# Optimization experiments

Measured on AMD Instinct MI355X. Metric: run time of the kernel, lower is better.

## Reference

```python
import jax, jax.numpy as jnp
import numpy as np

# Mamba-1.4B-like dims
BATCH, SEQ, HID = 1, 2048, 2048
INTER, STATE, DT_RANK, KCONV = 4096, 16, 128, 4


def setup_inputs() -> dict:
    key = jax.random.key(0)
    ks = jax.random.split(key, 8)
    f = jnp.float32
    return {
        "input_states": jax.random.normal(ks[0], (BATCH, SEQ, HID), f),
        "in_proj_w": jax.random.normal(ks[1], (HID, 2 * INTER), f) * (HID ** -0.5),
        "conv_w": jax.random.normal(ks[2], (INTER, 1, KCONV), f) * (KCONV ** -0.5),  # (O, I/groups=1, K) depthwise
        "conv_b": jnp.zeros((INTER,), f),
        "x_proj_w": jax.random.normal(ks[3], (INTER, DT_RANK + 2 * STATE), f) * (INTER ** -0.5),
        "dt_proj_w": jax.random.normal(ks[4], (DT_RANK, INTER), f) * (DT_RANK ** -0.5),
        "dt_proj_b": jax.random.normal(ks[5], (INTER,), f) * 0.1,
        "A_log": jnp.log(jnp.broadcast_to(jnp.arange(1, STATE + 1, dtype=f), (INTER, STATE))),
        "D": jnp.ones((INTER,), f),
        "out_proj_w": jax.random.normal(ks[6], (INTER, HID), f) * (INTER ** -0.5),
    }


def _mamba_forward(input_states, in_proj_w, conv_w, conv_b, x_proj_w,
                   dt_proj_w, dt_proj_b, A_log, D, out_proj_w):
    Bsz, L, _ = input_states.shape
    Idim, _, K = conv_w.shape
    N = A_log.shape[1]
    R = dt_proj_w.shape[0]

    proj = input_states @ in_proj_w                       # (B, L, 2I)
    hidden, gate = jnp.split(proj, 2, axis=-1)            # each (B, L, I)

    # depthwise causal conv over sequence (pad K-1, keep first L outputs)
    xc = jnp.swapaxes(hidden, 1, 2)                       # (B, I, L)
    xc = jax.lax.conv_general_dilated(
        xc, conv_w, window_strides=(1,), padding=((K - 1, K - 1),),
        feature_group_count=Idim)
    xc = xc[:, :, :L] + conv_b[None, :, None]
    u = jax.nn.silu(jnp.swapaxes(xc, 1, 2))               # (B, L, I)

    # input-dependent SSM params
    ssm_in = u @ x_proj_w                                 # (B, L, R + 2N)
    dt_in, Bc, Cc = jnp.split(ssm_in, [R, R + N], axis=-1)
    dt = jax.nn.softplus(dt_in @ dt_proj_w + dt_proj_b)   # (B, L, I)
    A = -jnp.exp(A_log)                                   # (I, N)

    def step(state, xs):
        dt_t, B_t, C_t, u_t = xs                          # (B,I) (B,N) (B,N) (B,I)
        dA = jnp.exp(dt_t[:, :, None] * A[None])          # (B, I, N)
        state = state * dA + (dt_t * u_t)[:, :, None] * B_t[:, None, :]
        y_t = jnp.einsum('bin,bn->bi', state, C_t)
        return state, y_t

    xs = (jnp.swapaxes(dt, 0, 1), jnp.swapaxes(Bc, 0, 1),
          jnp.swapaxes(Cc, 0, 1), jnp.swapaxes(u, 0, 1))
    state0 = jnp.zeros((Bsz, Idim, N), dt.dtype)
    _, ys = jax.lax.scan(step, state0, xs)                # (L, B, I)
    y = jnp.swapaxes(ys, 0, 1)                            # (B, L, I)

    y = (y + u * D) * jax.nn.silu(gate)
    return y @ out_proj_w                                 # (B, L, H)


def reference(input_states, in_proj_w, conv_w, conv_b, x_proj_w,
              dt_proj_w, dt_proj_b, A_log, D, out_proj_w):
    return _mamba_forward(input_states, in_proj_w, conv_w, conv_b, x_proj_w,
                          dt_proj_w, dt_proj_b, A_log, D, out_proj_w)
```

## Files before the change

kernel.cpp:

```cpp
#include <hip/hip_runtime.h>
#include <stdint.h>

#define LSEQ 2048
#define HID  2048
#define IDIM 4096
#define NSTATE 16
#define RRANK 128
#define GDIM 160

#define GCHUNK 64
#define TCHUNK (LSEQ / GCHUNK)

typedef _Float16 f16x8 __attribute__((ext_vector_type(8)));
typedef float f32x4 __attribute__((ext_vector_type(4)));

#define GLOAD_LDS16(g, l) __builtin_amdgcn_global_load_lds( \
    (const __attribute__((address_space(1))) void*)(g),     \
    (__attribute__((address_space(3))) void*)(l), 16, 0, 0)

__global__ void f32_to_f16_kernel(const float* __restrict__ in, _Float16* __restrict__ out, int n) {
    int i = blockIdx.x * 256 + threadIdx.x;
    if (i < n) out[i] = (_Float16)in[i];
}

__global__ void transpose_f32_f16_kernel(const float* __restrict__ in, _Float16* __restrict__ out,
                                         int R, int C) {
    __shared__ float tile[32][33];
    int bx = blockIdx.x;
    int by = blockIdx.y;
    int tx = threadIdx.x & 31;
    int ty = threadIdx.x >> 5;
    int r0 = by * 32, c0 = bx * 32;
    #pragma unroll
    for (int j = 0; j < 32; j += 8)
        tile[ty + j][tx] = in[(long)(r0 + ty + j) * C + c0 + tx];
    __syncthreads();
    #pragma unroll
    for (int j = 0; j < 32; j += 8)
        out[(long)(c0 + ty + j) * R + r0 + tx] = (_Float16)tile[tx][ty + j];
}

#define BM 128
#define BK 64

template <typename CT, int BN_>
__global__ __launch_bounds__(256)
void gemm_bt_kernel(const _Float16* __restrict__ A, const _Float16* __restrict__ Bt,
                    CT* __restrict__ C, int M, int N, int K, int kc) {
    constexpr int NI = BN_ / 32;
    constexpr int NISS_B = BN_ * 8 / 256;
    __shared__ _Float16 As[BM * BK];
    __shared__ _Float16 Bs[BN_ * BK];
    const int m0 = blockIdx.y * BM;
    const int n0 = blockIdx.x * BN_;
    const int t = threadIdx.x;
    const int wave = t >> 6;
    const int lane = t & 63;
    const int wm = wave >> 1, wn = wave & 1;
    const int lrow = lane & 15;
    const int quad = lane >> 4;
    const int sw8 = (lrow & 7) * 8;

    f32x4 acc[4][NI];
    #pragma unroll
    for (int mi = 0; mi < 4; ++mi)
        #pragma unroll
        for (int ni = 0; ni < NI; ++ni)
            #pragma unroll
            for (int r = 0; r < 4; ++r)
                acc[mi][ni][r] = 0.f;

    long gA[4];
    #pragma unroll
    for (int j = 0; j < 4; ++j) {
        int s = j * 256 + t;
        int row = s >> 3;
        int ch = (s & 7) ^ (row & 7);
        gA[j] = (long)(m0 + row) * K + ch * 8;
    }
    long gB[NISS_B];
    #pragma unroll
    for (int j = 0; j < NISS_B; ++j) {
        int s = j * 256 + t;
        int row = s >> 3;
        int ch = (s & 7) ^ (row & 7);
        gB[j] = (long)(n0 + row) * K + ch * 8;
    }

    const int k_begin = blockIdx.z * kc;
    const int k_end = k_begin + kc;

    for (int kk = k_begin; kk < k_end; kk += BK) {
        #pragma unroll
        for (int j = 0; j < 4; ++j)
            GLOAD_LDS16(A + gA[j] + kk, As + (j * 256 + wave * 64) * 8);
        #pragma unroll
        for (int j = 0; j < NISS_B; ++j)
            GLOAD_LDS16(Bt + gB[j] + kk, Bs + (j * 256 + wave * 64) * 8);
        __syncthreads();

        #pragma unroll
        for (int h = 0; h < 2; ++h) {
            const int qoff = (h * 32 + quad * 8) ^ sw8;
            f16x8 af[4], bf[NI];
            #pragma unroll
            for (int mi = 0; mi < 4; ++mi)
                af[mi] = *(const f16x8*)(As + (wm * 64 + mi * 16 + lrow) * BK + qoff);
            #pragma unroll
            for (int ni = 0; ni < NI; ++ni)
                bf[ni] = *(const f16x8*)(Bs + (wn * (BN_ / 2) + ni * 16 + lrow) * BK + qoff);
            #pragma unroll
            for (int mi = 0; mi < 4; ++mi)
                #pragma unroll
                for (int ni = 0; ni < NI; ++ni)
                    acc[mi][ni] = __builtin_amdgcn_mfma_f32_16x16x32_f16(af[mi], bf[ni], acc[mi][ni], 0, 0, 0);
        }
        __syncthreads();
    }

    CT* Cz = C + (long)blockIdx.z * M * N;
    #pragma unroll
    for (int mi = 0; mi < 4; ++mi) {
        #pragma unroll
        for (int ni = 0; ni < NI; ++ni) {
            int col = n0 + wn * (BN_ / 2) + ni * 16 + lrow;
            if (col < N) {
                #pragma unroll
                for (int r = 0; r < 4; ++r) {
                    int row = m0 + wm * 64 + mi * 16 + quad * 4 + r;
                    Cz[(long)row * N + col] = (CT)acc[mi][ni][r];
                }
            }
        }
    }
}

__global__ void xproj_reduce_kernel(const float* __restrict__ part, float* __restrict__ ssm,
                                    _Float16* __restrict__ dtin) {
    int idx = blockIdx.x * 256 + threadIdx.x;
    if (idx >= LSEQ * GDIM) return;
    int t = idx / GDIM;
    int c = idx - t * GDIM;
    float v = 0.f;
    #pragma unroll
    for (int k = 0; k < 8; ++k)
        v += part[((long)k * LSEQ + t) * 256 + c];
    ssm[idx] = v;
    if (c < RRANK) dtin[t * RRANK + c] = (_Float16)v;
}

__global__ void conv_silu_kernel(const _Float16* __restrict__ proj, const float* __restrict__ w,
                                 const float* __restrict__ b, _Float16* __restrict__ u16) {
    int idx = blockIdx.x * 256 + threadIdx.x;
    int i0 = (idx & 511) * 8;
    int t0 = (idx >> 9) * 4;
    f16x8 r[7];
    #pragma unroll
    for (int k = 0; k < 7; ++k) {
        int tt = t0 - 3 + k;
        if (tt >= 0) r[k] = *(const f16x8*)(proj + (long)tt * (2 * IDIM) + i0);
        else         r[k] = f16x8{0,0,0,0,0,0,0,0};
    }
    float4 wv[8]; float bb[8];
    #pragma unroll
    for (int j = 0; j < 8; ++j) { wv[j] = ((const float4*)w)[i0 + j]; bb[j] = b[i0 + j]; }
    #pragma unroll
    for (int tt = 0; tt < 4; ++tt) {
        f16x8 res;
        #pragma unroll
        for (int j = 0; j < 8; ++j) {
            float a = bb[j] + (float)r[tt][j] * wv[j].x + (float)r[tt+1][j] * wv[j].y
                            + (float)r[tt+2][j] * wv[j].z + (float)r[tt+3][j] * wv[j].w;
            res[j] = (_Float16)(a / (1.f + __expf(-a)));
        }
        *(f16x8*)(u16 + (long)(t0 + tt) * IDIM + i0) = res;
    }
}

__device__ __forceinline__ float softplus_f(float x) {
    if (x > 20.f) return x;
    return log1pf(__expf(x));
}
__device__ __forceinline__ float silu_f(float x) {
    return x / (1.f + __expf(-x));
}

__global__ __launch_bounds__(256)
void scan_pass1_kernel(const _Float16* __restrict__ dtlin, const float* __restrict__ dtb,
                       const float* __restrict__ ssm, const _Float16* __restrict__ u16,
                       const float* __restrict__ A_log,
                       float* __restrict__ Pc, float* __restrict__ Sc) {
    const int c = blockIdx.y;
    const int i = blockIdx.x * 256 + threadIdx.x;

    __shared__ float Bs[TCHUNK * 16];
    for (int idx = threadIdx.x; idx < TCHUNK * 16; idx += 256) {
        int t = idx >> 4, n = idx & 15;
        Bs[idx] = ssm[(c * TCHUNK + t) * GDIM + RRANK + n];
    }
    __syncthreads();

    float A[16];
    {
        const float4* Ap = (const float4*)(A_log + i * 16);
        #pragma unroll
        for (int q = 0; q < 4; ++q) {
            float4 v = Ap[q];
            A[q * 4 + 0] = -__expf(v.x);
            A[q * 4 + 1] = -__expf(v.y);
            A[q * 4 + 2] = -__expf(v.z);
            A[q * 4 + 3] = -__expf(v.w);
        }
    }
    const float dtbi = dtb[i];

    float s[16], p[16];
    #pragma unroll
    for (int n = 0; n < 16; ++n) { s[n] = 0.f; p[n] = 1.f; }

    long base = (long)c * TCHUNK * IDIM + i;
    for (int t = 0; t < TCHUNK; ++t) {
        float dt = softplus_f((float)dtlin[base + (long)t * IDIM] + dtbi);
        float dtu = dt * (float)u16[base + (long)t * IDIM];
        #pragma unroll
        for (int n = 0; n < 16; ++n) {
            float dA = __expf(dt * A[n]);
            s[n] = s[n] * dA + dtu * Bs[t * 16 + n];
            p[n] *= dA;
        }
    }

    long o = ((long)c * IDIM + i) * 16;
    #pragma unroll
    for (int q = 0; q < 4; ++q) {
        *(float4*)(Pc + o + q * 4) = make_float4(p[q*4+0], p[q*4+1], p[q*4+2], p[q*4+3]);
        *(float4*)(Sc + o + q * 4) = make_float4(s[q*4+0], s[q*4+1], s[q*4+2], s[q*4+3]);
    }
}

__global__ void scan_combine_kernel(const float* __restrict__ Pc, float* __restrict__ ScInit) {
    int tid = blockIdx.x * 256 + threadIdx.x;
    const long stride = (long)IDIM * 16;
    float p4[4], s4[4];
    #pragma unroll
    for (int k = 0; k < 4; ++k) {
        p4[k] = Pc[(long)k * stride + tid];
        s4[k] = ScInit[(long)k * stride + tid];
    }
    float carry = 0.f;
    for (int g = 0; g < GCHUNK / 4; ++g) {
        float pc[4], sc[4];
        #pragma unroll
        for (int k = 0; k < 4; ++k) { pc[k] = p4[k]; sc[k] = s4[k]; }
        if (g + 1 < GCHUNK / 4) {
            #pragma unroll
            for (int k = 0; k < 4; ++k) {
                long o2 = (long)((g + 1) * 4 + k) * stride + tid;
                p4[k] = Pc[o2];
                s4[k] = ScInit[o2];
            }
        }
        #pragma unroll
        for (int k = 0; k < 4; ++k) {
            long o = (long)(g * 4 + k) * stride + tid;
            ScInit[o] = carry;
            carry = carry * pc[k] + sc[k];
        }
    }
}

__global__ __launch_bounds__(256)
void scan_pass3_kernel(const _Float16* __restrict__ dtlin, const float* __restrict__ dtb,
                       const float* __restrict__ ssm, const _Float16* __restrict__ u16,
                       const _Float16* __restrict__ proj, const float* __restrict__ A_log,
                       const float* __restrict__ Dp, const float* __restrict__ Init,
                       _Float16* __restrict__ y16) {
    const int c = blockIdx.y;
    const int i = blockIdx.x * 256 + threadIdx.x;

    __shared__ float Bs[TCHUNK * 16];
    __shared__ float Cs[TCHUNK * 16];
    for (int idx = threadIdx.x; idx < TCHUNK * 16; idx += 256) {
        int t = idx >> 4, n = idx & 15;
        Bs[idx] = ssm[(c * TCHUNK + t) * GDIM + RRANK + n];
        Cs[idx] = ssm[(c * TCHUNK + t) * GDIM + RRANK + NSTATE + n];
    }
    __syncthreads();

    float A[16];
    {
        const float4* Ap = (const float4*)(A_log + i * 16);
        #pragma unroll
        for (int q = 0; q < 4; ++q) {
            float4 v = Ap[q];
            A[q * 4 + 0] = -__expf(v.x);
            A[q * 4 + 1] = -__expf(v.y);
            A[q * 4 + 2] = -__expf(v.z);
            A[q * 4 + 3] = -__expf(v.w);
        }
    }
    const float dtbi = dtb[i];
    const float Dv = Dp[i];

    float s[16];
    {
        long o = ((long)c * IDIM + i) * 16;
        #pragma unroll
        for (int q = 0; q < 4; ++q) {
            float4 v = *(const float4*)(Init + o + q * 4);
            s[q*4+0] = v.x; s[q*4+1] = v.y; s[q*4+2] = v.z; s[q*4+3] = v.w;
        }
    }

    long base = (long)c * TCHUNK * IDIM + i;
    for (int t = 0; t < TCHUNK; ++t) {
        float dt = softplus_f((float)dtlin[base + (long)t * IDIM] + dtbi);
        float uv = (float)u16[base + (long)t * IDIM];
        float dtu = dt * uv;
        float y = 0.f;
        #pragma unroll
        for (int n = 0; n < 16; ++n) {
            float dA = __expf(dt * A[n]);
            s[n] = s[n] * dA + dtu * Bs[t * 16 + n];
            y += s[n] * Cs[t * 16 + n];
        }
        int tg = c * TCHUNK + t;
        float g = (float)proj[(long)tg * (2 * IDIM) + IDIM + i];
        float out = (y + uv * Dv) * silu_f(g);
        y16[base + (long)t * IDIM] = (_Float16)out;
    }
}

extern "C" void kernel_launch(void* const* d_in, const int* in_sizes, int n_in,
                              void* d_out, int out_size, void* d_ws, size_t ws_size,
                              hipStream_t stream) {
    const float* x_in  = (const float*)d_in[0];
    const float* w_in  = (const float*)d_in[1];
    const float* cw    = (const float*)d_in[2];
    const float* cb    = (const float*)d_in[3];
    const float* xw    = (const float*)d_in[4];
    const float* dtw   = (const float*)d_in[5];
    const float* dtb   = (const float*)d_in[6];
    const float* alog  = (const float*)d_in[7];
    const float* Dp    = (const float*)d_in[8];
    const float* ow    = (const float*)d_in[9];
    float* out = (float*)d_out;

    char* p = (char*)d_ws;
    auto alloc = [&](size_t bytes) { char* r = p; p += (bytes + 255) & ~255ull; return r; };
    _Float16* Xf    = (_Float16*)alloc((size_t)LSEQ * HID * 2);
    _Float16* Wt1   = (_Float16*)alloc((size_t)2 * IDIM * HID * 2);
    _Float16* proj  = (_Float16*)alloc((size_t)LSEQ * 2 * IDIM * 2);
    _Float16* u16   = (_Float16*)alloc((size_t)LSEQ * IDIM * 2);
    _Float16* Wt2   = (_Float16*)alloc((size_t)256 * IDIM * 2);
    float*    ssm   = (float*)alloc((size_t)LSEQ * GDIM * 4);
    _Float16* dtin  = (_Float16*)alloc((size_t)LSEQ * RRANK * 2);
    _Float16* Wt3   = (_Float16*)alloc((size_t)IDIM * RRANK * 2);
    _Float16* dtlin = (_Float16*)alloc((size_t)LSEQ * IDIM * 2);
    _Float16* Wt4   = (_Float16*)alloc((size_t)HID * IDIM * 2);
    _Float16* y16   = (_Float16*)alloc((size_t)LSEQ * IDIM * 2);

    float* xpart = (float*)Wt1;
    float* Pc = (float*)Wt1;
    float* Sc = Pc + (size_t)GCHUNK * IDIM * 16;

    f32_to_f16_kernel<<<(LSEQ * HID) / 256, 256, 0, stream>>>(x_in, Xf, LSEQ * HID);
    transpose_f32_f16_kernel<<<dim3(2 * IDIM / 32, HID / 32), 256, 0, stream>>>(w_in, Wt1, HID, 2 * IDIM);
    transpose_f32_f16_kernel<<<dim3(GDIM / 32, IDIM / 32), 256, 0, stream>>>(xw, Wt2, IDIM, GDIM);
    transpose_f32_f16_kernel<<<dim3(IDIM / 32, RRANK / 32), 256, 0, stream>>>(dtw, Wt3, RRANK, IDIM);
    transpose_f32_f16_kernel<<<dim3(HID / 32, IDIM / 32), 256, 0, stream>>>(ow, Wt4, IDIM, HID);

    gemm_bt_kernel<_Float16, 128><<<dim3(2 * IDIM / 128, LSEQ / BM, 1), 256, 0, stream>>>(
        Xf, Wt1, proj, LSEQ, 2 * IDIM, HID, HID);
    conv_silu_kernel<<<(LSEQ / 4) * (IDIM / 8) / 256, 256, 0, stream>>>(proj, cw, cb, u16);
    gemm_bt_kernel<float, 128><<<dim3(2, LSEQ / BM, 8), 256, 0, stream>>>(
        u16, Wt2, xpart, LSEQ, 256, IDIM, IDIM / 8);
    xproj_reduce_kernel<<<(LSEQ * GDIM + 255) / 256, 256, 0, stream>>>(xpart, ssm, dtin);
    gemm_bt_kernel<_Float16, 128><<<dim3(IDIM / 128, LSEQ / BM, 1), 256, 0, stream>>>(
        dtin, Wt3, dtlin, LSEQ, IDIM, RRANK, RRANK);
    scan_pass1_kernel<<<dim3(IDIM / 256, GCHUNK), 256, 0, stream>>>(
        dtlin, dtb, ssm, u16, alog, Pc, Sc);
    scan_combine_kernel<<<(IDIM * NSTATE) / 256, 256, 0, stream>>>(Pc, Sc);
    scan_pass3_kernel<<<dim3(IDIM / 256, GCHUNK), 256, 0, stream>>>(
        dtlin, dtb, ssm, u16, proj, alog, Dp, Sc, y16);
    gemm_bt_kernel<float, 64><<<dim3(HID / 64, LSEQ / BM, 1), 256, 0, stream>>>(
        y16, Wt4, out, LSEQ, HID, IDIM, IDIM);
}
```

Baseline: 519.7 us.

## Vectorize weight transpose, use pointer increments in GEMM, split-K out_proj

```diff
diff --git a/kernel.cpp b/kernel.cpp
--- a/kernel.cpp
+++ b/kernel.cpp
@@ -23,21 +23,58 @@
     if (i < n) out[i] = (_Float16)in[i];
 }
 
-__global__ void transpose_f32_f16_kernel(const float* __restrict__ in, _Float16* __restrict__ out,
-                                         int R, int C) {
-    __shared__ float tile[32][33];
-    int bx = blockIdx.x;
-    int by = blockIdx.y;
-    int tx = threadIdx.x & 31;
-    int ty = threadIdx.x >> 5;
-    int r0 = by * 32, c0 = bx * 32;
-    #pragma unroll
-    for (int j = 0; j < 32; j += 8)
-        tile[ty + j][tx] = in[(long)(r0 + ty + j) * C + c0 + tx];
-    __syncthreads();
-    #pragma unroll
-    for (int j = 0; j < 32; j += 8)
-        out[(long)(c0 + ty + j) * R + r0 + tx] = (_Float16)tile[tx][ty + j];
+__global__ __launch_bounds__(256)
+void transpose_f32_f16_kernel(const float* __restrict__ in, _Float16* __restrict__ out,
+                              int R, int C) {
+    __shared__ _Float16 tile[64][66];
+    const int c0 = blockIdx.x * 64, r0 = blockIdx.y * 64;
+    const int t = threadIdx.x;
+    const int tx = t & 15, ty = t >> 4;
+    const int ox = t & 7, oy = t >> 3;
+    const bool full = (c0 + 64 <= C) && (r0 + 64 <= R);
+    if (full) {
+        #pragma unroll
+        for (int j = 0; j < 4; ++j) {
+            int r = ty + j * 16;
+            float4 v = *(const float4*)(in + (long)(r0 + r) * C + c0 + tx * 4);
+            tile[r][tx * 4 + 0] = (_Float16)v.x;
+            tile[r][tx * 4 + 1] = (_Float16)v.y;
+            tile[r][tx * 4 + 2] = (_Float16)v.z;
+            tile[r][tx * 4 + 3] = (_Float16)v.w;
+        }
+        __syncthreads();
+        #pragma unroll
+        for (int j = 0; j < 2; ++j) {
+            int c = oy + j * 32;
+            f16x8 v;
+            #pragma unroll
+            for (int e = 0; e < 8; ++e) v[e] = tile[ox * 8 + e][c];
+            *(f16x8*)(out + (long)(c0 + c) * R + r0 + ox * 8) = v;
+        }
+    } else {
+        #pragma unroll
+        for (int j = 0; j < 4; ++j) {
+            int r = ty + j * 16;
+            #pragma unroll
+            for (int e = 0; e < 4; ++e) {
+                int c = c0 + tx * 4 + e;
+                float v = (r0 + r < R && c < C) ? in[(long)(r0 + r) * C + c] : 0.f;
+                tile[r][tx * 4 + e] = (_Float16)v;
+            }
+        }
+        __syncthreads();
+        #pragma unroll
+        for (int j = 0; j < 2; ++j) {
+            int c = c0 + oy + j * 32;
+            if (c < C) {
+                #pragma unroll
+                for (int e = 0; e < 8; ++e) {
+                    int r = r0 + ox * 8 + e;
+                    if (r < R) out[(long)c * R + r] = tile[ox * 8 + e][oy + j * 32];
+                }
+            }
+        }
+    }
 }
 
 #define BM 128
@@ -70,33 +107,35 @@
             for (int r = 0; r < 4; ++r)
                 acc[mi][ni][r] = 0.f;
 
-    long gA[4];
+    const int k_begin = blockIdx.z * kc;
+    const _Float16* pA[4];
     #pragma unroll
     for (int j = 0; j < 4; ++j) {
         int s = j * 256 + t;
         int row = s >> 3;
         int ch = (s & 7) ^ (row & 7);
-        gA[j] = (long)(m0 + row) * K + ch * 8;
-    }
-    long gB[NISS_B];
+        pA[j] = A + (long)(m0 + row) * K + ch * 8 + k_begin;
+    }
+    const _Float16* pB[NISS_B];
     #pragma unroll
     for (int j = 0; j < NISS_B; ++j) {
         int s = j * 256 + t;
         int row = s >> 3;
         int ch = (s & 7) ^ (row & 7);
-        gB[j] = (long)(n0 + row) * K + ch * 8;
-    }
-
-    const int k_begin = blockIdx.z * kc;
-    const int k_end = k_begin + kc;
-
-    for (int kk = k_begin; kk < k_end; kk += BK) {
-        #pragma unroll
-        for (int j = 0; j < 4; ++j)
-            GLOAD_LDS16(A + gA[j] + kk, As + (j * 256 + wave * 64) * 8);
-        #pragma unroll
-        for (int j = 0; j < NISS_B; ++j)
-            GLOAD_LDS16(Bt + gB[j] + kk, Bs + (j * 256 + wave * 64) * 8);
+        pB[j] = Bt + (long)(n0 + row) * K + ch * 8 + k_begin;
+    }
+
+    for (int kk = 0; kk < kc; kk += BK) {
+        #pragma unroll
+        for (int j = 0; j < 4; ++j) {
+            GLOAD_LDS16(pA[j], As + (j * 256 + wave * 64) * 8);
+            pA[j] += BK;
+        }
+        #pragma unroll
+        for (int j = 0; j < NISS_B; ++j) {
+            GLOAD_LDS16(pB[j], Bs + (j * 256 + wave * 64) * 8);
+            pB[j] += BK;
+        }
         __syncthreads();
 
         #pragma unroll
@@ -147,6 +186,11 @@
         v += part[((long)k * LSEQ + t) * 256 + c];
     ssm[idx] = v;
     if (c < RRANK) dtin[t * RRANK + c] = (_Float16)v;
+}
+
+__global__ void opart_reduce_kernel(const float* __restrict__ part, float* __restrict__ out) {
+    int idx = blockIdx.x * 256 + threadIdx.x;
+    out[idx] = part[idx] + part[idx + (long)LSEQ * HID];
 }
 
 __global__ void conv_silu_kernel(const _Float16* __restrict__ proj, const float* __restrict__ w,
@@ -363,12 +407,13 @@
     float* xpart = (float*)Wt1;
     float* Pc = (float*)Wt1;
     float* Sc = Pc + (size_t)GCHUNK * IDIM * 16;
+    float* opart = (float*)Wt1;
 
     f32_to_f16_kernel<<<(LSEQ * HID) / 256, 256, 0, stream>>>(x_in, Xf, LSEQ * HID);
-    transpose_f32_f16_kernel<<<dim3(2 * IDIM / 32, HID / 32), 256, 0, stream>>>(w_in, Wt1, HID, 2 * IDIM);
-    transpose_f32_f16_kernel<<<dim3(GDIM / 32, IDIM / 32), 256, 0, stream>>>(xw, Wt2, IDIM, GDIM);
-    transpose_f32_f16_kernel<<<dim3(IDIM / 32, RRANK / 32), 256, 0, stream>>>(dtw, Wt3, RRANK, IDIM);
-    transpose_f32_f16_kernel<<<dim3(HID / 32, IDIM / 32), 256, 0, stream>>>(ow, Wt4, IDIM, HID);
+    transpose_f32_f16_kernel<<<dim3(2 * IDIM / 64, HID / 64), 256, 0, stream>>>(w_in, Wt1, HID, 2 * IDIM);
+    transpose_f32_f16_kernel<<<dim3((GDIM + 63) / 64, IDIM / 64), 256, 0, stream>>>(xw, Wt2, IDIM, GDIM);
+    transpose_f32_f16_kernel<<<dim3(IDIM / 64, RRANK / 64), 256, 0, stream>>>(dtw, Wt3, RRANK, IDIM);
+    transpose_f32_f16_kernel<<<dim3(HID / 64, IDIM / 64), 256, 0, stream>>>(ow, Wt4, IDIM, HID);
 
     gemm_bt_kernel<_Float16, 128><<<dim3(2 * IDIM / 128, LSEQ / BM, 1), 256, 0, stream>>>(
         Xf, Wt1, proj, LSEQ, 2 * IDIM, HID, HID);
@@ -383,6 +428,7 @@
     scan_combine_kernel<<<(IDIM * NSTATE) / 256, 256, 0, stream>>>(Pc, Sc);
     scan_pass3_kernel<<<dim3(IDIM / 256, GCHUNK), 256, 0, stream>>>(
         dtlin, dtb, ssm, u16, proj, alog, Dp, Sc, y16);
-    gemm_bt_kernel<float, 64><<<dim3(HID / 64, LSEQ / BM, 1), 256, 0, stream>>>(
-        y16, Wt4, out, LSEQ, HID, IDIM, IDIM);
-}
+    gemm_bt_kernel<float, 128><<<dim3(HID / 128, LSEQ / BM, 2), 256, 0, stream>>>(
+        y16, Wt4, opart, LSEQ, HID, IDIM, IDIM / 2);
+    opart_reduce_kernel<<<(LSEQ * HID) / 256, 256, 0, stream>>>(opart, out);
+}
```

After: 502.1 us. -3.4%, faster.
